# Kernel optimization log

Hardware: AMD Instinct MI355X
Metric: run time of the kernel (lower is better)

## Reference

```python
import jax, jax.numpy as jnp
import numpy as np

B, L, M, H = 16, 1024, 1024, 128
NEG = -1e30


def setup_inputs() -> dict:
    key = jax.random.key(0)
    ks = jax.random.split(key, 8)
    return {
        "text": jax.random.normal(ks[0], (B, L, H), dtype=jnp.float32),
        "modality": jax.random.normal(ks[1], (B, M, H), dtype=jnp.float32),
        "text_mask": jax.random.randint(ks[2], (B, L), 0, 2, dtype=jnp.int32),
        "modality_mask": jax.random.randint(ks[3], (B, M), 0, 2, dtype=jnp.int32),
        # learned parameters (xavier-uniform style scale)
        "text_weight": jax.random.normal(ks[4], (H, 1), dtype=jnp.float32) * 0.1,
        "modality_weight": jax.random.normal(ks[5], (H, 1), dtype=jnp.float32) * 0.1,
        "text_modality_weight": jax.random.normal(ks[6], (1, 1, H), dtype=jnp.float32) * 0.1,
        "bias": jnp.zeros((1,), dtype=jnp.float32),
    }


def reference(text, modality, text_mask, modality_mask,
              text_weight, modality_weight, text_modality_weight, bias):
    # similarity matrix s: (B, L, M)   (eval mode: dropout is identity)
    s0 = jnp.matmul(text, text_weight)                      # (B, L, 1)
    s1 = jnp.swapaxes(jnp.matmul(modality, modality_weight), 1, 2)  # (B, 1, M)
    s2 = jnp.einsum('blh,bmh->blm', text * text_modality_weight, modality)
    s = s0 + s1 + s2 + bias                                 # (B, L, M)

    mmask = modality_mask[:, None, :].astype(jnp.float32)   # (B, 1, M)
    tmask = text_mask[:, :, None].astype(jnp.float32)       # (B, L, 1)
    p1 = jax.nn.softmax(mmask * s + (1.0 - mmask) * NEG, axis=2)  # text->modality
    p2 = jax.nn.softmax(tmask * s + (1.0 - tmask) * NEG, axis=1)  # modality->text

    a = jnp.matmul(p1, modality)                            # (B, L, H)
    b = jnp.matmul(jnp.matmul(p1, jnp.swapaxes(p2, 1, 2)), text)  # (B, L, H)
    return jnp.concatenate([text, a, text * a, text * b], axis=2)  # (B, L, 8H)
```

## Files before the change

### kernel.cpp

```cpp
#include <hip/hip_runtime.h>

#define B_ 16
#define L_ 1024
#define M_ 1024
#define H_ 128

typedef unsigned short u16;
typedef unsigned int u32;
typedef __bf16 bf16x8 __attribute__((ext_vector_type(8)));
typedef float f32x4 __attribute__((ext_vector_type(4)));

__device__ __forceinline__ u16 f2bf(float x){
  u32 u = __float_as_uint(x);
  u = (u + 0x7fffu + ((u >> 16) & 1u)) >> 16;
  return (u16)u;
}

__global__ __launch_bounds__(256) void zero_f32(float4* __restrict__ p, int n4)
{
  int i = blockIdx.x * 256 + threadIdx.x;
  int stride = gridDim.x * 256;
  for (; i < n4; i += stride) p[i] = make_float4(0.f, 0.f, 0.f, 0.f);
}

__global__ __launch_bounds__(256) void prep_rows(
    const float* __restrict__ src, const float* __restrict__ dotw,
    const float* __restrict__ mulw, u16* __restrict__ outbf,
    float* __restrict__ dotout, int nrows)
{
  int row = blockIdx.x * 4 + (threadIdx.x >> 6);
  int lane = threadIdx.x & 63;
  if (row >= nrows) return;
  const float* r = src + (size_t)row * H_;
  float2 x = *(const float2*)&r[lane * 2];
  float2 wv = *(const float2*)&dotw[lane * 2];
  float d = x.x * wv.x + x.y * wv.y;
  #pragma unroll
  for (int off = 32; off; off >>= 1) d += __shfl_xor(d, off);
  float2 mv = mulw ? *(const float2*)&mulw[lane * 2] : make_float2(1.f, 1.f);
  u32 packed = (u32)f2bf(x.x * mv.x) | ((u32)f2bf(x.y * mv.y) << 16);
  ((u32*)outbf)[(size_t)row * 64 + lane] = packed;
  if (lane == 0) dotout[row] = d;
}

__global__ __launch_bounds__(256) void transpose_bf(
    const float* __restrict__ srcA, const float* __restrict__ srcB,
    const int* __restrict__ maskA, const int* __restrict__ maskB,
    u16* __restrict__ dstA, u16* __restrict__ dstB)
{
  int b = blockIdx.z & 15, sel = blockIdx.z >> 4;
  const float* src = (sel ? srcB : srcA) + (size_t)b * L_ * H_;
  const int* msk = (sel ? maskB : maskA) + b * 1024;
  u16* dst = (sel ? dstB : dstA) + (size_t)b * H_ * L_;
  int r0 = blockIdx.x * 64, h0 = blockIdx.y * 64;
  __shared__ u16 tile[64][65];
  int t = threadIdx.x;
  int j = t & 63, i0 = t >> 6;
  #pragma unroll
  for (int p = 0; p < 16; p++) {
    int i = i0 + p * 4;
    tile[i][j] = msk[r0 + i] ? f2bf(src[(size_t)(r0 + i) * H_ + h0 + j]) : (u16)0;
  }
  __syncthreads();
  int ii = (t & 15) * 4, jj0 = t >> 4;
  #pragma unroll
  for (int q = 0; q < 4; q++) {
    int jj = jj0 + q * 16;
    u32 lo = (u32)tile[ii][jj] | ((u32)tile[ii + 1][jj] << 16);
    u32 hi = (u32)tile[ii + 2][jj] | ((u32)tile[ii + 3][jj] << 16);
    uint2 pk; pk.x = lo; pk.y = hi;
    *(uint2*)&dst[(size_t)(h0 + jj) * L_ + r0 + ii] = pk;
  }
}

__global__ __launch_bounds__(256) void gemm_exp(
    const u16* __restrict__ A, const u16* __restrict__ Bm,
    const float* __restrict__ t0, const float* __restrict__ s1m,
    const float* __restrict__ bias, const int* __restrict__ tmask,
    const int* __restrict__ mmask, float* __restrict__ rowsum,
    float* __restrict__ colsum, u16* __restrict__ ET)
{
  int f = blockIdx.x;
  int orig = (f & 7) * 256 + (f >> 3);
  int b = orig >> 7;
  int a0 = (orig & 15) * 64, b0 = ((orig >> 4) & 7) * 128;
  int tid = threadIdx.x, lane = tid & 63, wid = tid >> 6;
  int wr = wid >> 1, wc = wid & 1;
  int c = lane & 15, q = lane >> 4;
  __shared__ __align__(16) char smem[24576];
  const u16* Ab = A + (size_t)(b * L_ + a0) * H_;
  const u16* Bb = Bm + (size_t)(b * M_ + b0) * H_;
  f32x4 acc[2][4];
  #pragma unroll
  for (int i = 0; i < 2; i++)
    #pragma unroll
    for (int j = 0; j < 4; j++) acc[i][j] = (f32x4){0.f, 0.f, 0.f, 0.f};
  for (int kt = 0; kt < 2; kt++) {
    __syncthreads();
    #pragma unroll
    for (int i = 0; i < 2; i++) {
      int cc = tid + 256 * i;
      int row = cc >> 3, col8 = cc & 7;
      uint4 v = *(const uint4*)(Ab + (size_t)row * H_ + kt * 64 + col8 * 8);
      *(uint4*)(smem + row * 128 + ((col8 * 16) ^ ((row & 7) << 4))) = v;
    }
    #pragma unroll
    for (int i = 0; i < 4; i++) {
      int cc = tid + 256 * i;
      int row = cc >> 3, col8 = cc & 7;
      uint4 v = *(const uint4*)(Bb + (size_t)row * H_ + kt * 64 + col8 * 8);
      *(uint4*)(smem + 8192 + row * 128 + ((col8 * 16) ^ ((row & 7) << 4))) = v;
    }
    __syncthreads();
    #pragma unroll
    for (int kk = 0; kk < 2; kk++) {
      int kbyte = kk * 64 + (q << 4);
      bf16x8 af[2], bfr[4];
      #pragma unroll
      for (int i = 0; i < 2; i++) {
        int ra = wr * 32 + i * 16 + c;
        af[i] = *(const bf16x8*)(smem + ra * 128 + (kbyte ^ ((ra & 7) << 4)));
      }
      #pragma unroll
      for (int j = 0; j < 4; j++) {
        int rb = wc * 64 + j * 16 + c;
        bfr[j] = *(const bf16x8*)(smem + 8192 + rb * 128 + (kbyte ^ ((rb & 7) << 4)));
      }
      #pragma unroll
      for (int i = 0; i < 2; i++)
        #pragma unroll
        for (int j = 0; j < 4; j++)
          acc[i][j] = __builtin_amdgcn_mfma_f32_16x16x32_bf16(af[i], bfr[j], acc[i][j], 0, 0, 0);
    }
  }
  float biasv = bias[0];
  float t0v[2][4];
  int tmv[2][4];
  #pragma unroll
  for (int i = 0; i < 2; i++)
    #pragma unroll
    for (int r = 0; r < 4; r++) {
      int ar = a0 + wr * 32 + i * 16 + q * 4 + r;
      t0v[i][r] = t0[b * L_ + ar];
      tmv[i][r] = tmask[b * L_ + ar];
    }
  float s1v[4];
  int mmv[4];
  #pragma unroll
  for (int j = 0; j < 4; j++) {
    int gcol = b0 + wc * 64 + j * 16 + c;
    s1v[j] = s1m[b * M_ + gcol];
    mmv[j] = mmask[b * M_ + gcol];
  }
  float ev[2][4][4];
  #pragma unroll
  for (int i = 0; i < 2; i++)
    #pragma unroll
    for (int j = 0; j < 4; j++)
      #pragma unroll
      for (int r = 0; r < 4; r++)
        ev[i][j][r] = __expf(acc[i][j][r] + t0v[i][r] + s1v[j] + biasv);
  #pragma unroll
  for (int i = 0; i < 2; i++)
    #pragma unroll
    for (int r = 0; r < 4; r++) {
      float prs = 0.f;
      #pragma unroll
      for (int j = 0; j < 4; j++) prs += mmv[j] ? ev[i][j][r] : 0.f;
      #pragma unroll
      for (int off = 1; off < 16; off <<= 1) prs += __shfl_xor(prs, off);
      if (c == 0) {
        int ar = a0 + wr * 32 + i * 16 + q * 4 + r;
        atomicAdd(&rowsum[b * L_ + ar], prs);
      }
    }
  #pragma unroll
  for (int j = 0; j < 4; j++) {
    float pcs = 0.f;
    #pragma unroll
    for (int i = 0; i < 2; i++)
      #pragma unroll
      for (int r = 0; r < 4; r++) pcs += tmv[i][r] ? ev[i][j][r] : 0.f;
    pcs += __shfl_xor(pcs, 16);
    pcs += __shfl_xor(pcs, 32);
    if (q == 0) {
      int gcol = b0 + wc * 64 + j * 16 + c;
      atomicAdd(&colsum[b * M_ + gcol], pcs);
    }
  }
  __syncthreads();
  u16* et = (u16*)smem;
  #pragma unroll
  for (int i = 0; i < 2; i++)
    #pragma unroll
    for (int j = 0; j < 4; j++) {
      int gcolL = wc * 64 + j * 16 + c;
      int arL = wr * 32 + i * 16 + q * 4;
      u32 lo = (u32)f2bf(ev[i][j][0]) | ((u32)f2bf(ev[i][j][1]) << 16);
      u32 hi = (u32)f2bf(ev[i][j][2]) | ((u32)f2bf(ev[i][j][3]) << 16);
      uint2 pk; pk.x = lo; pk.y = hi;
      *(uint2*)&et[gcolL * 72 + arL] = pk;
    }
  __syncthreads();
  #pragma unroll
  for (int it = 0; it < 4; it++) {
    int mrow = (tid >> 3) + it * 32;
    int l8 = tid & 7;
    uint4 v = *(const uint4*)&et[mrow * 72 + l8 * 8];
    *(uint4*)&ET[((size_t)(b * M_ + b0 + mrow)) * L_ + a0 + l8 * 8] = v;
  }
}

__global__ __launch_bounds__(512) void gemm_ct(
    const u16* __restrict__ A, const u16* __restrict__ ET,
    float* __restrict__ c_f32)
{
  int f = blockIdx.x;
  int orig = (f & 7) * 64 + (f >> 3);
  int b = orig >> 5;
  int x = orig & 3, y = (orig >> 2) & 7;
  int ia = x & 1, ks = x >> 1;
  int a0 = ia * 64, b0 = y * 128;
  int tid = threadIdx.x, lane = tid & 63, wid = tid >> 6;
  int wr = wid >> 2, wc = wid & 3;
  int c = lane & 15, q = lane >> 4;
  __shared__ __align__(16) char smem[24576];
  const u16* Ab = A + (size_t)(b * H_ + a0) * L_;
  const u16* Bb = ET + (size_t)(b * M_ + b0) * L_;
  f32x4 acc[2][2];
  #pragma unroll
  for (int i = 0; i < 2; i++)
    #pragma unroll
    for (int j = 0; j < 2; j++) acc[i][j] = (f32x4){0.f, 0.f, 0.f, 0.f};
  for (int kt = ks * 8; kt < ks * 8 + 8; kt++) {
    __syncthreads();
    {
      int row = tid >> 3, col8 = tid & 7;
      uint4 v = *(const uint4*)(Ab + (size_t)row * L_ + kt * 64 + col8 * 8);
      *(uint4*)(smem + row * 128 + ((col8 * 16) ^ ((row & 7) << 4))) = v;
    }
    #pragma unroll
    for (int i = 0; i < 2; i++) {
      int cc = tid + 512 * i;
      int row = cc >> 3, col8 = cc & 7;
      uint4 v = *(const uint4*)(Bb + (size_t)row * L_ + kt * 64 + col8 * 8);
      *(uint4*)(smem + 8192 + row * 128 + ((col8 * 16) ^ ((row & 7) << 4))) = v;
    }
    __syncthreads();
    #pragma unroll
    for (int kk = 0; kk < 2; kk++) {
      int kbyte = kk * 64 + (q << 4);
      bf16x8 af[2], bfr[2];
      #pragma unroll
      for (int i = 0; i < 2; i++) {
        int ra = wr * 32 + i * 16 + c;
        af[i] = *(const bf16x8*)(smem + ra * 128 + (kbyte ^ ((ra & 7) << 4)));
      }
      #pragma unroll
      for (int j = 0; j < 2; j++) {
        int rb = wc * 32 + j * 16 + c;
        bfr[j] = *(const bf16x8*)(smem + 8192 + rb * 128 + (kbyte ^ ((rb & 7) << 4)));
      }
      #pragma unroll
      for (int i = 0; i < 2; i++)
        #pragma unroll
        for (int j = 0; j < 2; j++)
          acc[i][j] = __builtin_amdgcn_mfma_f32_16x16x32_bf16(af[i], bfr[j], acc[i][j], 0, 0, 0);
    }
  }
  #pragma unroll
  for (int i = 0; i < 2; i++)
    #pragma unroll
    for (int j = 0; j < 2; j++) {
      int arow0 = a0 + wr * 32 + i * 16 + q * 4;
      int gcol = b0 + wc * 32 + j * 16 + c;
      #pragma unroll
      for (int r = 0; r < 4; r++)
        atomicAdd(&c_f32[((size_t)(b * H_ + arow0 + r)) * M_ + gcol], acc[i][j][r]);
    }
}

__global__ __launch_bounds__(256) void norm_ct(
    const float* __restrict__ c_f32, const float* __restrict__ colsum,
    const int* __restrict__ mmask, u16* __restrict__ cT)
{
  int g = blockIdx.x * 256 + threadIdx.x;
  int base = g * 4;
  int b = base >> 17;
  int m = base & (M_ - 1);
  float4 v = *(const float4*)&c_f32[base];
  float4 cs = *(const float4*)&colsum[b * M_ + m];
  int4 mm = *(const int4*)&mmask[b * M_ + m];
  float o0 = mm.x ? v.x / fmaxf(cs.x, 1e-30f) : 0.f;
  float o1 = mm.y ? v.y / fmaxf(cs.y, 1e-30f) : 0.f;
  float o2 = mm.z ? v.z / fmaxf(cs.z, 1e-30f) : 0.f;
  float o3 = mm.w ? v.w / fmaxf(cs.w, 1e-30f) : 0.f;
  uint2 pk;
  pk.x = (u32)f2bf(o0) | ((u32)f2bf(o1) << 16);
  pk.y = (u32)f2bf(o2) | ((u32)f2bf(o3) << 16);
  *(uint2*)&cT[base] = pk;
}

__global__ __launch_bounds__(512) void gemm_ab(
    const u16* __restrict__ ET, const u16* __restrict__ B1,
    const u16* __restrict__ B2, const float* __restrict__ rowsum,
    const float* __restrict__ text, float* __restrict__ out)
{
  int f = blockIdx.x;
  int orig = (f & 7) * 32 + (f >> 3);
  int b = orig >> 4;
  int a0 = (orig & 15) * 64;
  int tid = threadIdx.x, lane = tid & 63, wid = tid >> 6;
  int wr = wid >> 2, wc = wid & 3;
  int c = lane & 15, q = lane >> 4;
  __shared__ __align__(16) u16 At[64 * 76];
  __shared__ __align__(16) char Bs[2][16384];
  const u16* ETb = ET + (size_t)b * M_ * L_;
  const u16* B1b = B1 + (size_t)b * H_ * M_;
  const u16* B2b = B2 + (size_t)b * H_ * M_;
  f32x4 acc_a[2][2], acc_b[2][2];
  #pragma unroll
  for (int i = 0; i < 2; i++)
    #pragma unroll
    for (int j = 0; j < 2; j++) {
      acc_a[i][j] = (f32x4){0.f, 0.f, 0.f, 0.f};
      acc_b[i][j] = (f32x4){0.f, 0.f, 0.f, 0.f};
    }
  for (int kt = 0; kt < 16; kt++) {
    __syncthreads();
    {
      int mloc = tid >> 3, l8 = tid & 7;
      uint4 v = *(const uint4*)&ETb[((size_t)(kt * 64 + mloc)) * L_ + a0 + l8 * 8];
      u16* rp = At + mloc * 76 + l8 * 8;
      uint2 p0; p0.x = v.x; p0.y = v.y;
      uint2 p1; p1.x = v.z; p1.y = v.w;
      *(uint2*)rp = p0;
      *(uint2*)(rp + 4) = p1;
    }
    #pragma unroll
    for (int i = 0; i < 2; i++) {
      int cc = tid + 512 * i;
      int row = cc >> 3, col8 = cc & 7;
      uint4 v1 = *(const uint4*)(B1b + (size_t)row * M_ + kt * 64 + col8 * 8);
      *(uint4*)(Bs[0] + row * 128 + ((col8 * 16) ^ ((row & 7) << 4))) = v1;
      uint4 v2 = *(const uint4*)(B2b + (size_t)row * M_ + kt * 64 + col8 * 8);
      *(uint4*)(Bs[1] + row * 128 + ((col8 * 16) ^ ((row & 7) << 4))) = v2;
    }
    __syncthreads();
    #pragma unroll
    for (int kk = 0; kk < 2; kk++) {
      int kbyte = kk * 64 + (q << 4);
      bf16x8 af[2], b1f[2], b2f[2];
      #pragma unroll
      for (int i = 0; i < 2; i++) {
        int lidx = wr * 32 + i * 16 + c;
        int mbase = kk * 32 + q * 8;
        union { unsigned short s[8]; bf16x8 v; } ua;
        #pragma unroll
        for (int e = 0; e < 8; e++) ua.s[e] = At[(mbase + e) * 76 + lidx];
        af[i] = ua.v;
      }
      #pragma unroll
      for (int j = 0; j < 2; j++) {
        int rb = wc * 32 + j * 16 + c;
        b1f[j] = *(const bf16x8*)(Bs[0] + rb * 128 + (kbyte ^ ((rb & 7) << 4)));
        b2f[j] = *(const bf16x8*)(Bs[1] + rb * 128 + (kbyte ^ ((rb & 7) << 4)));
      }
      #pragma unroll
      for (int i = 0; i < 2; i++)
        #pragma unroll
        for (int j = 0; j < 2; j++) {
          acc_a[i][j] = __builtin_amdgcn_mfma_f32_16x16x32_bf16(af[i], b1f[j], acc_a[i][j], 0, 0, 0);
          acc_b[i][j] = __builtin_amdgcn_mfma_f32_16x16x32_bf16(af[i], b2f[j], acc_b[i][j], 0, 0, 0);
        }
    }
  }
  float irs[2][4];
  #pragma unroll
  for (int i = 0; i < 2; i++)
    #pragma unroll
    for (int r = 0; r < 4; r++) {
      int ar = a0 + wr * 32 + i * 16 + q * 4 + r;
      irs[i][r] = 1.0f / fmaxf(rowsum[b * L_ + ar], 1e-30f);
    }
  #pragma unroll
  for (int i = 0; i < 2; i++)
    #pragma unroll
    for (int j = 0; j < 2; j++) {
      int gcol = wc * 32 + j * 16 + c;
      #pragma unroll
      for (int r = 0; r < 4; r++) {
        int ar = a0 + wr * 32 + i * 16 + q * 4 + r;
        float av = acc_a[i][j][r] * irs[i][r];
        float bv = acc_b[i][j][r] * irs[i][r];
        float tv = text[((size_t)(b * L_ + ar)) * H_ + gcol];
        size_t base = ((size_t)(b * L_ + ar)) * 512 + gcol;
        out[base] = tv;
        out[base + 128] = av;
        out[base + 256] = tv * av;
        out[base + 384] = tv * bv;
      }
    }
}

extern "C" void kernel_launch(void* const* d_in, const int* in_sizes, int n_in,
                              void* d_out, int out_size, void* d_ws, size_t ws_size,
                              hipStream_t stream) {
  const float* text = (const float*)d_in[0];
  const float* modality = (const float*)d_in[1];
  const int* text_mask = (const int*)d_in[2];
  const int* modality_mask = (const int*)d_in[3];
  const float* text_weight = (const float*)d_in[4];
  const float* modality_weight = (const float*)d_in[5];
  const float* tmw = (const float*)d_in[6];
  const float* bias = (const float*)d_in[7];
  float* out = (float*)d_out;
  (void)in_sizes; (void)n_in; (void)out_size; (void)ws_size;

  char* ws = (char*)d_ws;
  size_t off = 0;
  auto alloc = [&](size_t bytes) { void* p = ws + off; off += (bytes + 255) & ~(size_t)255; return p; };
  u16*   ET       = (u16*)  alloc((size_t)B_ * M_ * L_ * 2);
  u16*   textw_bf = (u16*)  alloc((size_t)B_ * L_ * H_ * 2);
  u16*   mod_bf   = (u16*)  alloc((size_t)B_ * M_ * H_ * 2);
  u16*   textT_bf = (u16*)  alloc((size_t)B_ * H_ * L_ * 2);
  u16*   mod_bfT  = (u16*)  alloc((size_t)B_ * H_ * M_ * 2);
  u16*   cT       = (u16*)  alloc((size_t)B_ * H_ * M_ * 2);
  float* t0       = (float*)alloc((size_t)B_ * L_ * 4);
  float* s1m      = (float*)alloc((size_t)B_ * M_ * 4);
  float* rowsum   = (float*)alloc((size_t)B_ * L_ * 4);
  float* colsum   = (float*)alloc((size_t)B_ * M_ * 4);
  float* c_f32    = (float*)alloc((size_t)B_ * H_ * M_ * 4);

  int n4 = (B_ * (L_ + M_) + B_ * H_ * M_) / 4;
  zero_f32<<<2048, 256, 0, stream>>>((float4*)rowsum, n4);
  prep_rows<<<4096, 256, 0, stream>>>(text, text_weight, tmw, textw_bf, t0, B_ * L_);
  prep_rows<<<4096, 256, 0, stream>>>(modality, modality_weight, nullptr, mod_bf, s1m, B_ * M_);
  transpose_bf<<<dim3(16, 2, 32), 256, 0, stream>>>(text, modality, text_mask, modality_mask,
                                                    textT_bf, mod_bfT);
  gemm_exp<<<2048, 256, 0, stream>>>(textw_bf, mod_bf, t0, s1m, bias,
      text_mask, modality_mask, rowsum, colsum, ET);
  gemm_ct<<<512, 512, 0, stream>>>(textT_bf, ET, c_f32);
  norm_ct<<<2048, 256, 0, stream>>>(c_f32, colsum, modality_mask, cT);
  gemm_ab<<<256, 512, 0, stream>>>(ET, mod_bfT, cT, rowsum, text, out);
}
```

Measured before the change: 177.2 us.

## Fuse row prep with transpose and fold column normalization into gemm_ab

Merges the two prep_rows launches and transpose_bf into one prep2 kernel, which reads text and modality once and writes the bf16 row copies, the dot products and the masked transposes. It also removes norm_ct: gemm_ab now precomputes inverse column sums in shared memory and scales and converts c_f32 to bf16 while loading its B2 tile. This cuts three kernel launches and one read-write round trip of the cT buffer. In exchange gemm_ab reads fp32 data (twice the bytes of bf16) in its inner loop and uses 4 KB more shared memory.

```diff
diff --git a/kernel.cpp b/kernel.cpp
--- a/kernel.cpp
+++ b/kernel.cpp
@@ -23,53 +23,63 @@
   for (; i < n4; i += stride) p[i] = make_float4(0.f, 0.f, 0.f, 0.f);
 }
 
-__global__ __launch_bounds__(256) void prep_rows(
-    const float* __restrict__ src, const float* __restrict__ dotw,
-    const float* __restrict__ mulw, u16* __restrict__ outbf,
-    float* __restrict__ dotout, int nrows)
+__global__ __launch_bounds__(256) void prep2(
+    const float* __restrict__ text, const float* __restrict__ modality,
+    const int* __restrict__ tmask, const int* __restrict__ mmask,
+    const float* __restrict__ tw, const float* __restrict__ mw,
+    const float* __restrict__ tmw,
+    u16* __restrict__ textw_bf, u16* __restrict__ mod_bf,
+    u16* __restrict__ textT_bf, u16* __restrict__ modT_bf,
+    float* __restrict__ t0, float* __restrict__ s1m)
 {
-  int row = blockIdx.x * 4 + (threadIdx.x >> 6);
-  int lane = threadIdx.x & 63;
-  if (row >= nrows) return;
-  const float* r = src + (size_t)row * H_;
-  float2 x = *(const float2*)&r[lane * 2];
-  float2 wv = *(const float2*)&dotw[lane * 2];
-  float d = x.x * wv.x + x.y * wv.y;
-  #pragma unroll
-  for (int off = 32; off; off >>= 1) d += __shfl_xor(d, off);
-  float2 mv = mulw ? *(const float2*)&mulw[lane * 2] : make_float2(1.f, 1.f);
-  u32 packed = (u32)f2bf(x.x * mv.x) | ((u32)f2bf(x.y * mv.y) << 16);
-  ((u32*)outbf)[(size_t)row * 64 + lane] = packed;
-  if (lane == 0) dotout[row] = d;
-}
-
-__global__ __launch_bounds__(256) void transpose_bf(
-    const float* __restrict__ srcA, const float* __restrict__ srcB,
-    const int* __restrict__ maskA, const int* __restrict__ maskB,
-    u16* __restrict__ dstA, u16* __restrict__ dstB)
-{
-  int b = blockIdx.z & 15, sel = blockIdx.z >> 4;
-  const float* src = (sel ? srcB : srcA) + (size_t)b * L_ * H_;
-  const int* msk = (sel ? maskB : maskA) + b * 1024;
-  u16* dst = (sel ? dstB : dstA) + (size_t)b * H_ * L_;
-  int r0 = blockIdx.x * 64, h0 = blockIdx.y * 64;
-  __shared__ u16 tile[64][65];
-  int t = threadIdx.x;
-  int j = t & 63, i0 = t >> 6;
-  #pragma unroll
-  for (int p = 0; p < 16; p++) {
-    int i = i0 + p * 4;
-    tile[i][j] = msk[r0 + i] ? f2bf(src[(size_t)(r0 + i) * H_ + h0 + j]) : (u16)0;
+  int g = blockIdx.x;
+  int sel = g >> 8;
+  int b = (g >> 4) & 15;
+  int r0 = (g & 15) * 64;
+  const float* src = (sel ? modality : text) + ((size_t)b * 1024 + r0) * H_;
+  const int* msk = (sel ? mmask : tmask) + b * 1024 + r0;
+  const float* dotw = sel ? mw : tw;
+  u16* rowout = (sel ? mod_bf : textw_bf) + ((size_t)b * 1024 + r0) * H_;
+  u16* trout = (sel ? modT_bf : textT_bf) + (size_t)b * H_ * 1024 + r0;
+  float* dotout = (sel ? s1m : t0) + b * 1024 + r0;
+
+  __shared__ u16 tile[128][72];
+  int tid = threadIdx.x;
+  int rgrp = tid >> 5;
+  int lane32 = tid & 31;
+  int h0 = lane32 * 4;
+  float4 w4 = *(const float4*)&dotw[h0];
+  float4 mv = sel ? make_float4(1.f, 1.f, 1.f, 1.f) : *(const float4*)&tmw[h0];
+  float dpart[8];
+  #pragma unroll
+  for (int p = 0; p < 8; p++) {
+    int row = rgrp + p * 8;
+    float4 x = *(const float4*)&src[(size_t)row * H_ + h0];
+    dpart[p] = x.x * w4.x + x.y * w4.y + x.z * w4.z + x.w * w4.w;
+    uint2 pk;
+    pk.x = (u32)f2bf(x.x * mv.x) | ((u32)f2bf(x.y * mv.y) << 16);
+    pk.y = (u32)f2bf(x.z * mv.z) | ((u32)f2bf(x.w * mv.w) << 16);
+    *(uint2*)&rowout[(size_t)row * H_ + h0] = pk;
+    int mk = msk[row];
+    tile[h0 + 0][row] = mk ? f2bf(x.x) : (u16)0;
+    tile[h0 + 1][row] = mk ? f2bf(x.y) : (u16)0;
+    tile[h0 + 2][row] = mk ? f2bf(x.z) : (u16)0;
+    tile[h0 + 3][row] = mk ? f2bf(x.w) : (u16)0;
+  }
+  #pragma unroll
+  for (int p = 0; p < 8; p++) {
+    float d = dpart[p];
+    #pragma unroll
+    for (int off = 1; off < 32; off <<= 1) d += __shfl_xor(d, off);
+    if (lane32 == 0) dotout[rgrp + p * 8] = d;
   }
   __syncthreads();
-  int ii = (t & 15) * 4, jj0 = t >> 4;
-  #pragma unroll
-  for (int q = 0; q < 4; q++) {
-    int jj = jj0 + q * 16;
-    u32 lo = (u32)tile[ii][jj] | ((u32)tile[ii + 1][jj] << 16);
-    u32 hi = (u32)tile[ii + 2][jj] | ((u32)tile[ii + 3][jj] << 16);
-    uint2 pk; pk.x = lo; pk.y = hi;
-    *(uint2*)&dst[(size_t)(h0 + jj) * L_ + r0 + ii] = pk;
+  int lcol = (tid & 7) * 8;
+  #pragma unroll
+  for (int p = 0; p < 4; p++) {
+    int h = (tid >> 3) + p * 32;
+    uint4 v = *(const uint4*)&tile[h][lcol];
+    *(uint4*)&trout[(size_t)h * 1024 + lcol] = v;
   }
 }
 
@@ -280,30 +290,10 @@
     }
 }
 
-__global__ __launch_bounds__(256) void norm_ct(
-    const float* __restrict__ c_f32, const float* __restrict__ colsum,
-    const int* __restrict__ mmask, u16* __restrict__ cT)
-{
-  int g = blockIdx.x * 256 + threadIdx.x;
-  int base = g * 4;
-  int b = base >> 17;
-  int m = base & (M_ - 1);
-  float4 v = *(const float4*)&c_f32[base];
-  float4 cs = *(const float4*)&colsum[b * M_ + m];
-  int4 mm = *(const int4*)&mmask[b * M_ + m];
-  float o0 = mm.x ? v.x / fmaxf(cs.x, 1e-30f) : 0.f;
-  float o1 = mm.y ? v.y / fmaxf(cs.y, 1e-30f) : 0.f;
-  float o2 = mm.z ? v.z / fmaxf(cs.z, 1e-30f) : 0.f;
-  float o3 = mm.w ? v.w / fmaxf(cs.w, 1e-30f) : 0.f;
-  uint2 pk;
-  pk.x = (u32)f2bf(o0) | ((u32)f2bf(o1) << 16);
-  pk.y = (u32)f2bf(o2) | ((u32)f2bf(o3) << 16);
-  *(uint2*)&cT[base] = pk;
-}
-
 __global__ __launch_bounds__(512) void gemm_ab(
     const u16* __restrict__ ET, const u16* __restrict__ B1,
-    const u16* __restrict__ B2, const float* __restrict__ rowsum,
+    const float* __restrict__ c_f32, const float* __restrict__ colsum,
+    const int* __restrict__ mmask, const float* __restrict__ rowsum,
     const float* __restrict__ text, float* __restrict__ out)
 {
   int f = blockIdx.x;
@@ -315,9 +305,12 @@
   int c = lane & 15, q = lane >> 4;
   __shared__ __align__(16) u16 At[64 * 76];
   __shared__ __align__(16) char Bs[2][16384];
+  __shared__ float invcm[1024];
   const u16* ETb = ET + (size_t)b * M_ * L_;
   const u16* B1b = B1 + (size_t)b * H_ * M_;
-  const u16* B2b = B2 + (size_t)b * H_ * M_;
+  const float* cfb = c_f32 + (size_t)b * H_ * M_;
+  for (int i = tid; i < 1024; i += 512)
+    invcm[i] = mmask[b * M_ + i] ? 1.0f / fmaxf(colsum[b * M_ + i], 1e-30f) : 0.f;
   f32x4 acc_a[2][2], acc_b[2][2];
   #pragma unroll
   for (int i = 0; i < 2; i++)
@@ -343,7 +336,16 @@
       int row = cc >> 3, col8 = cc & 7;
       uint4 v1 = *(const uint4*)(B1b + (size_t)row * M_ + kt * 64 + col8 * 8);
       *(uint4*)(Bs[0] + row * 128 + ((col8 * 16) ^ ((row & 7) << 4))) = v1;
-      uint4 v2 = *(const uint4*)(B2b + (size_t)row * M_ + kt * 64 + col8 * 8);
+      int mbase = kt * 64 + col8 * 8;
+      float4 xa = *(const float4*)&cfb[(size_t)row * M_ + mbase];
+      float4 xb = *(const float4*)&cfb[(size_t)row * M_ + mbase + 4];
+      float4 ia4 = *(const float4*)&invcm[mbase];
+      float4 ib4 = *(const float4*)&invcm[mbase + 4];
+      uint4 v2;
+      v2.x = (u32)f2bf(xa.x * ia4.x) | ((u32)f2bf(xa.y * ia4.y) << 16);
+      v2.y = (u32)f2bf(xa.z * ia4.z) | ((u32)f2bf(xa.w * ia4.w) << 16);
+      v2.z = (u32)f2bf(xb.x * ib4.x) | ((u32)f2bf(xb.y * ib4.y) << 16);
+      v2.w = (u32)f2bf(xb.z * ib4.z) | ((u32)f2bf(xb.w * ib4.w) << 16);
       *(uint4*)(Bs[1] + row * 128 + ((col8 * 16) ^ ((row & 7) << 4))) = v2;
     }
     __syncthreads();
@@ -425,7 +427,6 @@
   u16*   mod_bf   = (u16*)  alloc((size_t)B_ * M_ * H_ * 2);
   u16*   textT_bf = (u16*)  alloc((size_t)B_ * H_ * L_ * 2);
   u16*   mod_bfT  = (u16*)  alloc((size_t)B_ * H_ * M_ * 2);
-  u16*   cT       = (u16*)  alloc((size_t)B_ * H_ * M_ * 2);
   float* t0       = (float*)alloc((size_t)B_ * L_ * 4);
   float* s1m      = (float*)alloc((size_t)B_ * M_ * 4);
   float* rowsum   = (float*)alloc((size_t)B_ * L_ * 4);
@@ -434,13 +435,12 @@
 
   int n4 = (B_ * (L_ + M_) + B_ * H_ * M_) / 4;
   zero_f32<<<2048, 256, 0, stream>>>((float4*)rowsum, n4);
-  prep_rows<<<4096, 256, 0, stream>>>(text, text_weight, tmw, textw_bf, t0, B_ * L_);
-  prep_rows<<<4096, 256, 0, stream>>>(modality, modality_weight, nullptr, mod_bf, s1m, B_ * M_);
-  transpose_bf<<<dim3(16, 2, 32), 256, 0, stream>>>(text, modality, text_mask, modality_mask,
-                                                    textT_bf, mod_bfT);
+  prep2<<<512, 256, 0, stream>>>(text, modality, text_mask, modality_mask,
+      text_weight, modality_weight, tmw,
+      textw_bf, mod_bf, textT_bf, mod_bfT, t0, s1m);
   gemm_exp<<<2048, 256, 0, stream>>>(textw_bf, mod_bf, t0, s1m, bias,
       text_mask, modality_mask, rowsum, colsum, ET);
   gemm_ct<<<512, 512, 0, stream>>>(textT_bf, ET, c_f32);
-  norm_ct<<<2048, 256, 0, stream>>>(c_f32, colsum, modality_mask, cT);
-  gemm_ab<<<256, 512, 0, stream>>>(ET, mod_bfT, cT, rowsum, text, out);
-}
+  gemm_ab<<<256, 512, 0, stream>>>(ET, mod_bfT, c_f32, colsum, modality_mask,
+      rowsum, text, out);
+}
```

Measured after the change: 181.2 us. 1.02x slower.
